# Optimization experiments

Measured on AMD Instinct MI355X. Metric: run time of the kernel, lower is better.

Reference implementation:

```python
import jax, jax.numpy as jnp
import numpy as np

B, T, C, H = 4, 2048, 1024, 16
D = C // H


def setup_inputs() -> dict:
    key = jax.random.key(0)
    ks = jax.random.split(key, 5)
    s = C ** -0.5  # keep linear outputs O(1) like standard init
    x = jax.random.normal(ks[0], (B, T, C), dtype=jnp.float32)
    Wq = jax.random.normal(ks[1], (C, C), dtype=jnp.float32) * s
    Wk = jax.random.normal(ks[2], (C, C), dtype=jnp.float32) * s
    Wv = jax.random.normal(ks[3], (C, C), dtype=jnp.float32) * s
    Wproj = jax.random.normal(ks[4], (C, C), dtype=jnp.float32) * s
    alpha_raw = jnp.zeros((1, H, 1, 1), dtype=jnp.float32)
    beta_raw = jnp.zeros((1, H, 1, 1), dtype=jnp.float32)
    state = jnp.zeros((B, H, D, D), dtype=jnp.float32)
    return dict(x=x, Wq=Wq, Wk=Wk, Wv=Wv, Wproj=Wproj,
                alpha_raw=alpha_raw, beta_raw=beta_raw, state=state)


def reference(x, Wq, Wk, Wv, Wproj, alpha_raw, beta_raw, state):
    Bx, Tx, Cx = x.shape
    Hn = alpha_raw.shape[1]
    Dh = Cx // Hn
    # projections (torch Linear: x @ W^T), split heads -> (B, H, T, D)
    def proj(W):
        return (x @ W.T).reshape(Bx, Tx, Hn, Dh).transpose(0, 2, 1, 3)
    q, k, v = proj(Wq), proj(Wk), proj(Wv)
    # F.normalize(k, dim=-1) with eps=1e-12
    k = k / jnp.maximum(jnp.linalg.norm(k, axis=-1, keepdims=True), 1e-12)
    alpha = jax.nn.sigmoid(alpha_raw) * 0.5  # (1, H, 1, 1)
    beta = jax.nn.sigmoid(beta_raw) * 0.5

    def step(st, qkv):
        qt, kt, vt = qkv  # each (B, H, D)
        # y_t = q_t @ state^T
        y = jnp.einsum('bhe,bhde->bhd', qt, st)
        # Mk = state @ k_t
        Mk = jnp.einsum('bhde,bhe->bhd', st, kt)
        st = st - alpha * jnp.einsum('bhd,bhe->bhde', Mk, kt) \
                + beta * jnp.einsum('bhd,bhe->bhde', vt, kt)
        return st, y

    # scan over time: (T, B, H, D)
    qT = q.transpose(2, 0, 1, 3)
    kT = k.transpose(2, 0, 1, 3)
    vT = v.transpose(2, 0, 1, 3)
    state_f, ys = jax.lax.scan(step, state, (qT, kT, vT))
    y = ys.transpose(1, 0, 2, 3).reshape(Bx, Tx, Cx)  # (B, T, C)
    out = y @ Wproj.T
    return out, state_f
```

## Files before the change

### kernel.cpp

```cpp
#include <hip/hip_runtime.h>
#include <hip/hip_bf16.h>
#include <cstdint>

#define B_ 4
#define T_ 2048
#define C_ 1024
#define H_ 16
#define D_ 64
#define NC_ 32
#define L_ 64

typedef __attribute__((ext_vector_type(8))) short bf16x8;
typedef __attribute__((ext_vector_type(4))) float f32x4;

static __device__ __forceinline__ unsigned short f2bf(float f) {
  unsigned u = __float_as_uint(f);
  u += 0x7fff + ((u >> 16) & 1);
  return (unsigned short)(u >> 16);
}
static __device__ __forceinline__ float bf2f(unsigned short b) {
  return __uint_as_float(((unsigned)b) << 16);
}
static __device__ __forceinline__ int swz128(int row, int byte) {
  return row * 128 + (byte ^ ((row & 7) << 4));
}

#define LDS_BARRIER() asm volatile("s_waitcnt lgkmcnt(0)\ns_barrier" ::: "memory")
#define VMCNT0 asm volatile("s_waitcnt vmcnt(0)" ::: "memory");

__global__ __launch_bounds__(256) void cvt_all(const float* __restrict__ x,
                                               const float* __restrict__ wq,
                                               const float* __restrict__ wk,
                                               const float* __restrict__ wv,
                                               const float* __restrict__ wp,
                                               unsigned short* __restrict__ xbf,
                                               unsigned short* __restrict__ W3,
                                               unsigned short* __restrict__ Wp) {
  const int bidx = blockIdx.x;
  const float* src;
  unsigned short* dst;
  long base;
  if (bidx < 8192) {
    src = x; dst = xbf; base = (long)bidx * 1024;
  } else {
    const int g = (bidx - 8192) >> 10;
    src = (g == 0) ? wq : (g == 1) ? wk : (g == 2) ? wv : wp;
    dst = (g < 3) ? (W3 + (long)g * 1048576) : Wp;
    base = (long)((bidx - 8192) & 1023) * 1024;
  }
  long i = base + threadIdx.x * 4;
  float4 v = *reinterpret_cast<const float4*>(src + i);
  ushort4 o;
  o.x = f2bf(v.x); o.y = f2bf(v.y); o.z = f2bf(v.z); o.w = f2bf(v.w);
  *reinterpret_cast<ushort4*>(dst + i) = o;
}


#define STAGEH(GP, GR0, KT, LOFF) do {                                            \
    const unsigned short* _s = (GP) + ((GR0) + wid * 8 + lr8) * 1024L             \
                               + (long)(KT) * 64 + skb * 8;                       \
    char* _d = (char*)lds + (LOFF) + wid * 1024;                                  \
    __builtin_amdgcn_global_load_lds((const __attribute__((address_space(1))) void*)_s,      \
        (__attribute__((address_space(3))) void*)_d, 16, 0, 0);                   \
    __builtin_amdgcn_global_load_lds((const __attribute__((address_space(1))) void*)(_s + 64 * 1024L), \
        (__attribute__((address_space(3))) void*)(_d + 8192), 16, 0, 0);          \
  } while (0)

#define PHASE4(AO, BO, NH, STG, ENDVM) do {                                       \
    bf16x8 av[4][2], bv[2][2];                                                    \
    {                                                                             \
      const char* ab = (const char*)lds + (AO) + arow;                            \
      const char* bb = (const char*)lds + (BO) + (NH) * 16384 + brow;             \
      _Pragma("unroll")                                                           \
      for (int j = 0; j < 4; ++j) {                                               \
        av[j][0] = *(const bf16x8*)(ab + j * 4096 + cb0);                         \
        av[j][1] = *(const bf16x8*)(ab + j * 4096 + cb1);                         \
      }                                                                           \
      _Pragma("unroll")                                                           \
      for (int j2 = 0; j2 < 2; ++j2) {                                            \
        bv[j2][0] = *(const bf16x8*)(bb + j2 * 8192 + cb0);                       \
        bv[j2][1] = *(const bf16x8*)(bb + j2 * 8192 + cb1);                       \
      }                                                                           \
    }                                                                             \
    STG;                                                                          \
    __builtin_amdgcn_s_barrier();                                                 \
    asm volatile("s_waitcnt lgkmcnt(0)" ::: "memory");                            \
    __builtin_amdgcn_sched_barrier(0);                                            \
    __builtin_amdgcn_s_setprio(1);                                                \
    _Pragma("unroll")                                                             \
    for (int j = 0; j < 4; ++j)                                                   \
      _Pragma("unroll")                                                           \
      for (int j2 = 0; j2 < 2; ++j2)                                              \
        acc[j][(NH) * 2 + j2] = __builtin_amdgcn_mfma_f32_16x16x32_bf16(          \
            av[j][0], bv[j2][0], acc[j][(NH) * 2 + j2], 0, 0, 0);                 \
    _Pragma("unroll")                                                             \
    for (int j = 0; j < 4; ++j)                                                   \
      _Pragma("unroll")                                                           \
      for (int j2 = 0; j2 < 2; ++j2)                                              \
        acc[j][(NH) * 2 + j2] = __builtin_amdgcn_mfma_f32_16x16x32_bf16(          \
            av[j][1], bv[j2][1], acc[j][(NH) * 2 + j2], 0, 0, 0);                 \
    __builtin_amdgcn_s_setprio(0);                                                \
    ENDVM                                                                         \
    __builtin_amdgcn_s_barrier();                                                 \
  } while (0)

template<int OUT_BF16>
__global__ __launch_bounds__(512, 2) void gemm128x256(
    const unsigned short* __restrict__ A,
    const unsigned short* __restrict__ Bw,
    void* __restrict__ Cp, int N) {
  __shared__ __align__(16) char lds[98304];
  enum { EA = 0, EB = 16384, OA = 49152, OB = 65536 };
  const int tid = threadIdx.x;
  const int wid = tid >> 6, lane = tid & 63;
  const int wm = wid >> 2, wn = wid & 3;
  const int f = lane & 15, g = lane >> 4;
  const int lr8 = lane >> 3, lc = lane & 7;
  const int skb = lc ^ lr8;
  const int bid = blockIdx.y * gridDim.x + blockIdx.x;
  const int cpx = (gridDim.x * gridDim.y) >> 3;
  const int sw = (bid & 7) * cpx + (bid >> 3);
  const long bM = (long)(sw / gridDim.x) * 128;
  const long bN = (long)(sw % gridDim.x) * 256;
  const int cb0 = ((0 + g) ^ (f & 7)) * 16;
  const int cb1 = ((4 + g) ^ (f & 7)) * 16;
  const int arow = (wm * 16 + f) * 128;
  const int brow = (wn * 16 + f) * 128;

  f32x4 acc[4][4] = {};

  STAGEH(Bw, bN, 0, EB);
  STAGEH(Bw, bN + 128, 0, EB + 16384);
  STAGEH(A, bM, 0, EA);
  VMCNT0
  __builtin_amdgcn_s_barrier();

  for (int i = 0; i < 8; ++i) {
    const int to = 2 * i + 1;
    const int te = 2 * i + 2;
    PHASE4(EA, EB, 0,
           { STAGEH(Bw, bN, to, OB); STAGEH(Bw, bN + 128, to, OB + 16384); STAGEH(A, bM, to, OA); },
           );
    PHASE4(EA, EB, 1, {}, VMCNT0);
    PHASE4(OA, OB, 0,
           { if (i < 7) { STAGEH(Bw, bN, te, EB); STAGEH(Bw, bN + 128, te, EB + 16384); STAGEH(A, bM, te, EA); } },
           );
    PHASE4(OA, OB, 1, {}, VMCNT0);
  }

#pragma unroll
  for (int mf = 0; mf < 4; ++mf) {
    long row = bM + mf * 32 + wm * 16 + g * 4;
#pragma unroll
    for (int nf = 0; nf < 4; ++nf) {
      long col = bN + (nf >> 1) * 128 + (nf & 1) * 64 + wn * 16 + f;
#pragma unroll
      for (int r = 0; r < 4; ++r) {
        if (OUT_BF16)
          ((unsigned short*)Cp)[(row + r) * (long)N + col] = f2bf(acc[mf][nf][r]);
        else
          ((float*)Cp)[(row + r) * (long)N + col] = acc[mf][nf][r];
      }
    }
  }
}

__global__ __launch_bounds__(256) void chunk_prep(
    unsigned short* __restrict__ qkv,
    const float* __restrict__ a_raw, const float* __restrict__ b_raw,
    unsigned short* __restrict__ Ubuf, unsigned short* __restrict__ Wbuf,
    unsigned short* __restrict__ SLbuf) {
  __shared__ __align__(16) unsigned short sK[64 * 64];
  __shared__ __align__(16) unsigned short sQ[64 * 64];
  __shared__ __align__(16) unsigned short sV[64 * 64];
  __shared__ float sA[64 * 64];

  const int blk = blockIdx.x;
  const int bh = blk >> 5, c = blk & 31;
  const int b = bh >> 4, h = bh & 15;
  const int tid = threadIdx.x;
  const int wid = tid >> 6, lane = tid & 63;

  const float alpha = 0.5f / (1.f + __expf(-a_raw[h]));
  const float beta  = 0.5f / (1.f + __expf(-b_raw[h]));

  {
    const int row = tid >> 2, cg = tid & 3;
    unsigned short* gp = qkv + (long)(b * 2048 + c * 64 + row) * 3072 + h * 64 + cg * 16;
    bf16x8 q0 = *(const bf16x8*)(gp);
    bf16x8 q1 = *(const bf16x8*)(gp + 8);
    bf16x8 k0 = *(const bf16x8*)(gp + 1024);
    bf16x8 k1 = *(const bf16x8*)(gp + 1024 + 8);
    bf16x8 v0 = *(const bf16x8*)(gp + 2048);
    bf16x8 v1 = *(const bf16x8*)(gp + 2048 + 8);
    float kf[16];
    float ss = 0.f;
#pragma unroll
    for (int i = 0; i < 8; ++i) { kf[i] = bf2f((unsigned short)k0[i]); ss += kf[i] * kf[i]; }
#pragma unroll
    for (int i = 0; i < 8; ++i) { kf[8 + i] = bf2f((unsigned short)k1[i]); ss += kf[8 + i] * kf[8 + i]; }
    ss += __shfl_xor(ss, 1);
    ss += __shfl_xor(ss, 2);
    const float inv = 1.f / fmaxf(sqrtf(ss), 1e-12f);
    bf16x8 n0, n1;
#pragma unroll
    for (int i = 0; i < 8; ++i) { n0[i] = (short)f2bf(kf[i] * inv); n1[i] = (short)f2bf(kf[8 + i] * inv); }
    *(bf16x8*)((char*)sK + swz128(row, cg * 32)) = n0;
    *(bf16x8*)((char*)sK + swz128(row, cg * 32 + 16)) = n1;
    *(bf16x8*)((char*)sQ + swz128(row, cg * 32)) = q0;
    *(bf16x8*)((char*)sQ + swz128(row, cg * 32 + 16)) = q1;
    *(bf16x8*)((char*)sV + row * 128 + cg * 32) = v0;
    *(bf16x8*)((char*)sV + row * 128 + cg * 32 + 16) = v1;
  }
  __syncthreads();

  {
    const int erow = tid >> 2, tq = tid & 3;
    unsigned short kt[16];
#pragma unroll
    for (int i = 0; i < 16; ++i)
      kt[i] = *(const unsigned short*)((const char*)sK + swz128(tq * 16 + i, 2 * erow));
    unsigned short* vp = qkv + (long)(b * 2048 + c * 64 + erow) * 3072 + 2048 + h * 64 + tq * 16;
    *(bf16x8*)vp = *(const bf16x8*)kt;
    *(bf16x8*)(vp + 8) = *(const bf16x8*)(kt + 8);
  }

  const int rfrag = lane & 15, koff = (lane >> 4) * 8, crow = (lane >> 4) * 4;
  const int w2 = wid & 1;
  if (wid < 2) {
#pragma unroll
    for (int mt = 0; mt < 2; ++mt) {
      const int m = w2 * 2 + mt;
      const int ra = 16 * m + rfrag;
      f32x4 acc[4] = {};
#pragma unroll
      for (int ks = 0; ks < 2; ++ks) {
        bf16x8 af = *(const bf16x8*)((const char*)sK + swz128(ra, ks * 64 + koff * 2));
#pragma unroll
        for (int n = 0; n < 4; ++n) {
          bf16x8 bf = *(const bf16x8*)((const char*)sK + swz128(16 * n + rfrag, ks * 64 + koff * 2));
          acc[n] = __builtin_amdgcn_mfma_f32_16x16x32_bf16(af, bf, acc[n], 0, 0, 0);
        }
      }
#pragma unroll
      for (int n = 0; n < 4; ++n)
#pragma unroll
        for (int r = 0; r < 4; ++r)
          sA[(16 * m + crow + r) * 64 + 16 * n + rfrag] = acc[n][r];
    }
  } else {
#pragma unroll
    for (int mt = 0; mt < 2; ++mt) {
      const int m = w2 * 2 + mt;
      const int ra = 16 * m + rfrag;
      f32x4 acc[4] = {};
#pragma unroll
      for (int ks = 0; ks < 2; ++ks) {
        bf16x8 af = *(const bf16x8*)((const char*)sQ + swz128(ra, ks * 64 + koff * 2));
#pragma unroll
        for (int n = 0; n < 4; ++n) {
          bf16x8 bf = *(const bf16x8*)((const char*)sK + swz128(16 * n + rfrag, ks * 64 + koff * 2));
          acc[n] = __builtin_amdgcn_mfma_f32_16x16x32_bf16(af, bf, acc[n], 0, 0, 0);
        }
      }
#pragma unroll
      for (int n = 0; n < 4; ++n)
#pragma unroll
        for (int r = 0; r < 4; ++r) {
          int t = 16 * m + crow + r, j = 16 * n + rfrag;
          SLbuf[(long)blk * 4096 + t * 64 + j] = (j < t) ? f2bf(acc[n][r]) : (unsigned short)0;
        }
    }
  }
  __syncthreads();

  if (wid < 2) {
    const int d = lane;
    float x[64];
#pragma unroll
    for (int t = 0; t < 64; ++t) {
      float rhs;
      if (wid == 0) rhs = beta * bf2f(sV[t * 64 + d]);
      else          rhs = alpha * bf2f(*(const unsigned short*)((const char*)sK + swz128(t, 2 * d)));
      float s = 0.f;
#pragma unroll
      for (int j = 0; j < t; ++j) s = fmaf(sA[t * 64 + j], x[j], s);
      x[t] = rhs - alpha * s;
    }
    unsigned short* ob = (wid == 0 ? Ubuf : Wbuf) + (long)blk * 4096 + d;
#pragma unroll
    for (int t = 0; t < 64; ++t) ob[t * 64] = f2bf(x[t]);
  }
}

__global__ __launch_bounds__(256) void chunk_scan(
    const unsigned short* __restrict__ qkv,
    const unsigned short* __restrict__ Ubuf, const unsigned short* __restrict__ Wbuf,
    const unsigned short* __restrict__ SLbuf,
    const float* __restrict__ state_in, unsigned short* __restrict__ ybuf,
    float* __restrict__ state_out) {
  __shared__ __align__(16) char lds[73728];

  const int bid0 = blockIdx.x;
  const int blk = (bid0 & 7) * 32 + (bid0 >> 3);
  const int bh = blk >> 2, dq = blk & 3;
  const int b = bh >> 4, h = bh & 15;
  const int tid = threadIdx.x, wid = tid >> 6, lane = tid & 63;
  const int rfrag = lane & 15, koff = (lane >> 4) * 8, crow = (lane >> 4) * 4;
  const int row = tid >> 2, cg = tid & 3;

  char* gt = lds + 69632;
  char* ssb = lds + 71680;

  const unsigned short* gpb = qkv + (long)(b * 2048 + row) * 3072 + h * 64 + cg * 16;
  const long tbb = ((long)(bh * 32) * 64 + row) * 64 + cg * 16;
  const long ubb = ((long)(bh * 32) * 64 + (tid >> 1)) * 64 + dq * 16 + (tid & 1) * 8;

  bf16x8 qv0, qv1, kt0, kt1, wv0, wv1, sl0, sl1, uv;
#define LOADREGS(CN) do {                                                       \
    const unsigned short* gp = gpb + (long)(CN) * 64 * 3072;                    \
    const long tb = tbb + (long)(CN) * 4096;                                    \
    qv0 = *(const bf16x8*)gp;            qv1 = *(const bf16x8*)(gp + 8);        \
    kt0 = *(const bf16x8*)(gp + 2048);   kt1 = *(const bf16x8*)(gp + 2048 + 8); \
    wv0 = *(const bf16x8*)(Wbuf + tb);   wv1 = *(const bf16x8*)(Wbuf + tb + 8); \
    sl0 = *(const bf16x8*)(SLbuf + tb);  sl1 = *(const bf16x8*)(SLbuf + tb + 8);\
    if (tid < 128) uv = *(const bf16x8*)(Ubuf + ubb + (long)(CN) * 4096);       \
  } while (0)

#define WRITE_TILES(BUF) do {                                                   \
    char* bp_ = lds + (BUF) * 34816;                                            \
    *(bf16x8*)(bp_ + swz128(row, cg * 32)) = qv0;                               \
    *(bf16x8*)(bp_ + swz128(row, cg * 32 + 16)) = qv1;                          \
    *(bf16x8*)(bp_ + 8192 + swz128(row, cg * 32)) = wv0;                        \
    *(bf16x8*)(bp_ + 8192 + swz128(row, cg * 32 + 16)) = wv1;                   \
    *(bf16x8*)(bp_ + 16384 + swz128(row, cg * 32)) = sl0;                       \
    *(bf16x8*)(bp_ + 16384 + swz128(row, cg * 32 + 16)) = sl1;                  \
    *(bf16x8*)(bp_ + 24576 + swz128(row, cg * 32)) = kt0;                       \
    *(bf16x8*)(bp_ + 24576 + swz128(row, cg * 32 + 16)) = kt1;                  \
    if (tid < 128) *(bf16x8*)(bp_ + 32768 + ((tid >> 1) * 16 + (tid & 1) * 8) * 2) = uv; \
  } while (0)

  f32x4 sacc;
#pragma unroll
  for (int r = 0; r < 4; ++r)
    sacc[r] = state_in[(long)bh * 4096 + (dq * 16 + crow + r) * 64 + 16 * wid + rfrag];
#pragma unroll
  for (int r = 0; r < 4; ++r)
    *(unsigned short*)(ssb + swz128(crow + r, 2 * (16 * wid + rfrag))) = f2bf(sacc[r]);

  LOADREGS(0);
  WRITE_TILES(0);
  LOADREGS(1);
  LDS_BARRIER();

  for (int c = 0; c < NC_; ++c) {
    const int cur = c & 1;
    const char* bp = lds + cur * 34816;
    const int ta = 16 * wid + rfrag;

    f32x4 p = {};
    f32x4 yac = {};
#pragma unroll
    for (int ks = 0; ks < 2; ++ks) {
      bf16x8 afw = *(const bf16x8*)(bp + 8192 + swz128(ta, ks * 64 + koff * 2));
      bf16x8 afq = *(const bf16x8*)(bp + swz128(ta, ks * 64 + koff * 2));
      bf16x8 bS = *(const bf16x8*)(ssb + swz128(rfrag, ks * 64 + koff * 2));
      p = __builtin_amdgcn_mfma_f32_16x16x32_bf16(afw, bS, p, 0, 0, 0);
      yac = __builtin_amdgcn_mfma_f32_16x16x32_bf16(afq, bS, yac, 0, 0, 0);
    }
#pragma unroll
    for (int r = 0; r < 4; ++r) {
      int t = 16 * wid + crow + r;
      float gg = bf2f(*(const unsigned short*)(bp + 32768 + (t * 16 + rfrag) * 2)) - p[r];
      *(unsigned short*)(gt + swz128(rfrag, 2 * t)) = f2bf(gg);
    }
    LDS_BARRIER();

#pragma unroll
    for (int ks = 0; ks < 2; ++ks) {
      bf16x8 aSL = *(const bf16x8*)(bp + 16384 + swz128(ta, ks * 64 + koff * 2));
      bf16x8 bGT = *(const bf16x8*)(gt + swz128(rfrag, ks * 64 + koff * 2));
      yac = __builtin_amdgcn_mfma_f32_16x16x32_bf16(aSL, bGT, yac, 0, 0, 0);
    }
#pragma unroll
    for (int ks = 0; ks < 2; ++ks) {
      bf16x8 aGT = *(const bf16x8*)(gt + swz128(rfrag, ks * 64 + koff * 2));
      bf16x8 bKT = *(const bf16x8*)(bp + 24576 + swz128(16 * wid + rfrag, ks * 64 + koff * 2));
      sacc = __builtin_amdgcn_mfma_f32_16x16x32_bf16(aGT, bKT, sacc, 0, 0, 0);
    }
#pragma unroll
    for (int r = 0; r < 4; ++r) {
      int t = 16 * wid + crow + r;
      ybuf[(long)(b * 2048 + c * 64 + t) * 1024 + h * 64 + dq * 16 + rfrag] = f2bf(yac[r]);
    }
#pragma unroll
    for (int r = 0; r < 4; ++r)
      *(unsigned short*)(ssb + swz128(crow + r, 2 * (16 * wid + rfrag))) = f2bf(sacc[r]);
    if (c + 1 < NC_) {
      WRITE_TILES(cur ^ 1);
      int cn = c + 2; if (cn > NC_ - 1) cn = NC_ - 1;
      LOADREGS(cn);
    }
    LDS_BARRIER();
  }

#pragma unroll
  for (int r = 0; r < 4; ++r)
    state_out[(long)bh * 4096 + (dq * 16 + crow + r) * 64 + 16 * wid + rfrag] = sacc[r];
#undef LOADREGS
#undef WRITE_TILES
}

extern "C" void kernel_launch(void* const* d_in, const int* in_sizes, int n_in,
                              void* d_out, int out_size, void* d_ws, size_t ws_size,
                              hipStream_t stream) {
  (void)in_sizes; (void)n_in; (void)out_size; (void)ws_size;
  const float* x     = (const float*)d_in[0];
  const float* Wq    = (const float*)d_in[1];
  const float* Wk    = (const float*)d_in[2];
  const float* Wv    = (const float*)d_in[3];
  const float* Wproj = (const float*)d_in[4];
  const float* a_raw = (const float*)d_in[5];
  const float* b_raw = (const float*)d_in[6];
  const float* state = (const float*)d_in[7];

  char* ws = (char*)d_ws;
  unsigned short* xbf = (unsigned short*)ws;
  unsigned short* W3  = (unsigned short*)(ws + (16l << 20));
  unsigned short* Wp  = (unsigned short*)(ws + (22l << 20));
  unsigned short* qkv = (unsigned short*)(ws + (24l << 20));
  unsigned short* Ub  = (unsigned short*)(ws + (72l << 20));
  unsigned short* Wb  = (unsigned short*)(ws + (88l << 20));
  unsigned short* SLb = (unsigned short*)(ws + (104l << 20));
  float* out = (float*)d_out;
  float* state_out = out + (long)B_ * T_ * C_;

  cvt_all<<<dim3(12288), dim3(256), 0, stream>>>(x, Wq, Wk, Wv, Wproj, xbf, W3, Wp);

  gemm128x256<1><<<dim3(3072 / 256, 8192 / 128), dim3(512), 0, stream>>>(xbf, W3, (void*)qkv, 3072);

  chunk_prep<<<dim3(2048), dim3(256), 0, stream>>>(qkv, a_raw, b_raw, Ub, Wb, SLb);
  chunk_scan<<<dim3(256), dim3(256), 0, stream>>>(qkv, Ub, Wb, SLb, state, xbf, state_out);

  gemm128x256<0><<<dim3(1024 / 256, 8192 / 128), dim3(512), 0, stream>>>(xbf, Wp, (void*)out, 1024);
}
```

Baseline: 176.6 us.

## Triple-buffer GEMM LDS stages to keep two k-tiles in flight

Replaces the double-buffered LDS ring in the 128x256 bf16 GEMM with a three-slot ring, prefetching tile t+2 while computing tile t. The vmcnt wait now drains only to 6 outstanding loads instead of 0, so global loads get more time to overlap with MFMA work. LDS use grows from 96KB to 144KB per block, which with 512 threads may drop occupancy to one block per CU despite launch_bounds(512,2). The tail issues redundant loads of tile 15 to keep the wait counts uniform.

```diff
diff --git a/kernel.cpp b/kernel.cpp
--- a/kernel.cpp
+++ b/kernel.cpp
@@ -26,7 +26,6 @@
 }
 
 #define LDS_BARRIER() asm volatile("s_waitcnt lgkmcnt(0)\ns_barrier" ::: "memory")
-#define VMCNT0 asm volatile("s_waitcnt vmcnt(0)" ::: "memory");
 
 __global__ __launch_bounds__(256) void cvt_all(const float* __restrict__ x,
                                                const float* __restrict__ wq,
@@ -66,11 +65,11 @@
         (__attribute__((address_space(3))) void*)(_d + 8192), 16, 0, 0);          \
   } while (0)
 
-#define PHASE4(AO, BO, NH, STG, ENDVM) do {                                       \
+#define PHASE3(RG, NH, STG, ENDVM) do {                                           \
     bf16x8 av[4][2], bv[2][2];                                                    \
     {                                                                             \
-      const char* ab = (const char*)lds + (AO) + arow;                            \
-      const char* bb = (const char*)lds + (BO) + (NH) * 16384 + brow;             \
+      const char* ab = (const char*)lds + (RG) + arow;                            \
+      const char* bb = (const char*)lds + (RG) + 16384 + (NH) * 16384 + brow;     \
       _Pragma("unroll")                                                           \
       for (int j = 0; j < 4; ++j) {                                               \
         av[j][0] = *(const bf16x8*)(ab + j * 4096 + cb0);                         \
@@ -109,8 +108,7 @@
     const unsigned short* __restrict__ A,
     const unsigned short* __restrict__ Bw,
     void* __restrict__ Cp, int N) {
-  __shared__ __align__(16) char lds[98304];
-  enum { EA = 0, EB = 16384, OA = 49152, OB = 65536 };
+  __shared__ __align__(16) char lds[147456];
   const int tid = threadIdx.x;
   const int wid = tid >> 6, lane = tid & 63;
   const int wm = wid >> 2, wn = wid & 3;
@@ -129,24 +127,27 @@
 
   f32x4 acc[4][4] = {};
 
-  STAGEH(Bw, bN, 0, EB);
-  STAGEH(Bw, bN + 128, 0, EB + 16384);
-  STAGEH(A, bM, 0, EA);
-  VMCNT0
+  STAGEH(Bw, bN, 0, 16384);
+  STAGEH(Bw, bN + 128, 0, 32768);
+  STAGEH(A, bM, 0, 0);
+  STAGEH(Bw, bN, 1, 49152 + 16384);
+  STAGEH(Bw, bN + 128, 1, 49152 + 32768);
+  STAGEH(A, bM, 1, 49152);
+  asm volatile("s_waitcnt vmcnt(6)" ::: "memory");
   __builtin_amdgcn_s_barrier();
 
-  for (int i = 0; i < 8; ++i) {
-    const int to = 2 * i + 1;
-    const int te = 2 * i + 2;
-    PHASE4(EA, EB, 0,
-           { STAGEH(Bw, bN, to, OB); STAGEH(Bw, bN + 128, to, OB + 16384); STAGEH(A, bM, to, OA); },
+#pragma unroll
+  for (int t = 0; t < 16; ++t) {
+    const int rg = (t % 3) * 49152;
+    const int ng = ((t + 2) % 3) * 49152;
+    const int ts = (t + 2 > 15) ? 15 : t + 2;
+    PHASE3(rg, 0,
+           { STAGEH(Bw, bN, ts, ng + 16384); STAGEH(Bw, bN + 128, ts, ng + 32768); STAGEH(A, bM, ts, ng); },
            );
-    PHASE4(EA, EB, 1, {}, VMCNT0);
-    PHASE4(OA, OB, 0,
-           { if (i < 7) { STAGEH(Bw, bN, te, EB); STAGEH(Bw, bN + 128, te, EB + 16384); STAGEH(A, bM, te, EA); } },
-           );
-    PHASE4(OA, OB, 1, {}, VMCNT0);
-  }
+    PHASE3(rg, 1, {},
+           asm volatile("s_waitcnt vmcnt(6)" ::: "memory"););
+  }
+  asm volatile("s_waitcnt vmcnt(0)" ::: "memory");
 
 #pragma unroll
   for (int mf = 0; mf < 4; ++mf) {
```

New measurement: 174.8 us. About the same (-1.0%).
